# Performance work log

Measured on AMD Instinct MI355X. Metric: run time of the kernel, lower is better.

Reference implementation:

```python
import jax, jax.numpy as jnp
import numpy as np

N, D, C, E, K = 100000, 64, 40, 1600000, 2

def setup_inputs() -> dict:
    key = jax.random.key(0)
    k1, k2, k3 = jax.random.split(key, 3)
    x = jax.random.normal(k1, (N, D), dtype=jnp.float32)
    edge_index = jax.random.randint(k2, (2, E), 0, N, dtype=jnp.int64)
    W = jax.random.normal(k3, (D, C), dtype=jnp.float32) * 0.05
    b = jnp.zeros((C,), dtype=jnp.float32)
    return {"x": x, "edge_index": edge_index, "W": W, "b": b}

def reference(x, edge_index, W, b):
    n = x.shape[0]
    self_loop = jnp.arange(n, dtype=edge_index.dtype)
    row = jnp.concatenate([edge_index[0], self_loop])  # [E+N]
    col = jnp.concatenate([edge_index[1], self_loop])  # [E+N]
    # degree over row (out-degree incl. self loops), as in torch_geometric.utils.degree
    deg = jax.ops.segment_sum(jnp.ones_like(row, dtype=x.dtype), row, num_segments=n)
    deg_inv_sqrt = jnp.where(deg > 0, jax.lax.rsqrt(deg), 0.0)
    norm = deg_inv_sqrt[row] * deg_inv_sqrt[col]  # [E+N]
    # K hops of SpMM: out[r] += norm_e * x[c] for each edge e=(r,c)
    for _ in range(K):
        x = jax.ops.segment_sum(norm[:, None] * x[col], row, num_segments=n)
    logits = x @ W + b  # [N, C]
    return jax.nn.log_softmax(logits, axis=1)
```

## Files before the change

### kernel.cpp

```cpp
#include <hip/hip_runtime.h>
#include <math.h>


#define D_FEAT 64
#define NCLS 40
#define BROWS 512
#define BROWS_LOG 9
#define BINCAP 10240
#define CSRCAP 12288
#define EPT 25

__device__ __forceinline__ unsigned pack_bf16_2(float lo, float hi) {
    unsigned ulo = __float_as_uint(lo);
    unsigned uhi = __float_as_uint(hi);
    ulo = (ulo + 0x7fffu + ((ulo >> 16) & 1u)) >> 16;
    uhi = (uhi + 0x7fffu + ((uhi >> 16) & 1u)) & 0xffff0000u;
    return uhi | ulo;
}

__device__ __forceinline__ void acc2(unsigned u, float& a, float& b) {
    a += __uint_as_float(u << 16);
    b += __uint_as_float(u & 0xffff0000u);
}

__global__ void zero_cursors_kernel(int* __restrict__ cur, int nb) {
    int i = blockIdx.x * blockDim.x + threadIdx.x;
    if (i < nb) cur[i] = 0;
}

__global__ __launch_bounds__(256) void bin_edges_kernel(const int* __restrict__ rows,
                                                        const int* __restrict__ cols,
                                                        int* __restrict__ bucket_cursor,
                                                        unsigned* __restrict__ bins,
                                                        int e, int nb) {
    __shared__ int cnt[512];
    for (int i = threadIdx.x; i < nb; i += 256) cnt[i] = 0;
    __syncthreads();
    int base = blockIdx.x * (256 * EPT) + threadIdx.x;
    int rr[EPT], cc[EPT];
#pragma unroll
    for (int k = 0; k < EPT; k++) {
        int idx = base + k * 256;
        if (idx < e) { rr[k] = rows[idx]; cc[k] = cols[idx]; }
        else { rr[k] = -1; cc[k] = 0; }
    }
#pragma unroll
    for (int k = 0; k < EPT; k++)
        if (rr[k] >= 0) atomicAdd(&cnt[rr[k] >> BROWS_LOG], 1);
    __syncthreads();
    for (int i = threadIdx.x; i < nb; i += 256) {
        int c = cnt[i];
        cnt[i] = (c > 0) ? atomicAdd(&bucket_cursor[i], c) : 0;
    }
    __syncthreads();
#pragma unroll
    for (int k = 0; k < EPT; k++) {
        if (rr[k] >= 0) {
            int b = rr[k] >> BROWS_LOG;
            int pos = atomicAdd(&cnt[b], 1);
            bins[(size_t)b * BINCAP + pos] =
                ((unsigned)(rr[k] & (BROWS - 1)) << 17) | (unsigned)cc[k];
        }
    }
}

__global__ __launch_bounds__(512) void build_csr_kernel(const unsigned* __restrict__ bins,
                                                        const int* __restrict__ bucket_cursor,
                                                        int* __restrict__ csr_col,
                                                        uint2* __restrict__ row_info,
                                                        float* __restrict__ dis, int n) {
    __shared__ int cnt[512];
    __shared__ int sm[512];
    __shared__ int cur[512];
    __shared__ int lcsr[CSRCAP];
    int b = blockIdx.x;
    int tid = threadIdx.x;
    int m = bucket_cursor[b];
    cnt[tid] = 0;
    __syncthreads();
    const unsigned* bp = bins + (size_t)b * BINCAP;
    for (int i = tid; i < m; i += 512) atomicAdd(&cnt[bp[i] >> 17], 1);
    __syncthreads();
    int c = cnt[tid];
    int padded = (c + 3) & ~3;
    int r = b * BROWS + tid;
    if (r < n) dis[r] = rsqrtf(1.0f + (float)c);
    sm[tid] = padded;
    __syncthreads();
    for (int off = 1; off < 512; off <<= 1) {
        int t = (tid >= off) ? sm[tid - off] : 0;
        __syncthreads();
        sm[tid] += t;
        __syncthreads();
    }
    int off0 = sm[tid] - padded;
    cur[tid] = off0;
    if (r < n) row_info[r] = make_uint2((unsigned)(b * CSRCAP + off0), (unsigned)padded);
    __syncthreads();
    for (int i = tid; i < m; i += 512) {
        unsigned u = bp[i];
        int pos = atomicAdd(&cur[u >> 17], 1);
        lcsr[pos] = (int)(u & 0x1FFFFu);
    }
    __syncthreads();
    for (int i2 = off0 + 1; i2 < off0 + c; i2++) {
        int key = lcsr[i2];
        int j = i2 - 1;
        while (j >= off0 && lcsr[j] > key) { lcsr[j + 1] = lcsr[j]; j--; }
        lcsr[j + 1] = key;
    }
    for (int j = off0 + c; j < off0 + padded; j++) lcsr[j] = n;
    __syncthreads();
    int tot = sm[511];
    int4* cp4 = (int4*)(csr_col + (size_t)b * CSRCAP);
    const int4* l4 = (const int4*)lcsr;
    for (int i = tid; i < (tot >> 2); i += 512) cp4[i] = l4[i];
}

__global__ void scale_x_kernel(const float* __restrict__ x, const float* __restrict__ dis,
                               unsigned* __restrict__ xs0, unsigned* __restrict__ xs1, int n) {
    int i = blockIdx.x * blockDim.x + threadIdx.x;
    int total = (n + 1) * (D_FEAT / 2);
    if (i >= total) return;
    int node = i >> 5;
    if (node < n) {
        float s = dis[node];
        float2 v = ((const float2*)x)[i];
        xs0[i] = pack_bf16_2(s * v.x, s * v.y);
    } else {
        xs0[i] = 0u;
        xs1[i] = 0u;
    }
}

#define GATHER16(cp, xs_in, ql, base, len)                                  \
    uint2 u0 = make_uint2(0u, 0u), u1 = u0, u2 = u0, u3 = u0;               \
    uint2 u4 = u0, u5 = u0, u6 = u0, u7 = u0;                               \
    uint2 u8 = u0, u9 = u0, u10 = u0, u11 = u0;                             \
    uint2 u12 = u0, u13 = u0, u14 = u0, u15 = u0;                           \
    if (base < len) {                                                       \
        uint4 cv = cp[(base >> 2) + 0];                                     \
        u0 = xs_in[cv.x * 16 + ql]; u1 = xs_in[cv.y * 16 + ql];             \
        u2 = xs_in[cv.z * 16 + ql]; u3 = xs_in[cv.w * 16 + ql];             \
    }                                                                       \
    if (base + 4 < len) {                                                   \
        uint4 cv = cp[(base >> 2) + 1];                                     \
        u4 = xs_in[cv.x * 16 + ql]; u5 = xs_in[cv.y * 16 + ql];             \
        u6 = xs_in[cv.z * 16 + ql]; u7 = xs_in[cv.w * 16 + ql];             \
    }                                                                       \
    if (base + 8 < len) {                                                   \
        uint4 cv = cp[(base >> 2) + 2];                                     \
        u8 = xs_in[cv.x * 16 + ql]; u9 = xs_in[cv.y * 16 + ql];             \
        u10 = xs_in[cv.z * 16 + ql]; u11 = xs_in[cv.w * 16 + ql];           \
    }                                                                       \
    if (base + 12 < len) {                                                  \
        uint4 cv = cp[(base >> 2) + 3];                                     \
        u12 = xs_in[cv.x * 16 + ql]; u13 = xs_in[cv.y * 16 + ql];           \
        u14 = xs_in[cv.z * 16 + ql]; u15 = xs_in[cv.w * 16 + ql];           \
    }                                                                       \
    acc2(u0.x, h0, h1); acc2(u0.y, h2, h3);                                 \
    acc2(u1.x, h0, h1); acc2(u1.y, h2, h3);                                 \
    acc2(u2.x, h0, h1); acc2(u2.y, h2, h3);                                 \
    acc2(u3.x, h0, h1); acc2(u3.y, h2, h3);                                 \
    acc2(u4.x, h0, h1); acc2(u4.y, h2, h3);                                 \
    acc2(u5.x, h0, h1); acc2(u5.y, h2, h3);                                 \
    acc2(u6.x, h0, h1); acc2(u6.y, h2, h3);                                 \
    acc2(u7.x, h0, h1); acc2(u7.y, h2, h3);                                 \
    acc2(u8.x, h0, h1); acc2(u8.y, h2, h3);                                 \
    acc2(u9.x, h0, h1); acc2(u9.y, h2, h3);                                 \
    acc2(u10.x, h0, h1); acc2(u10.y, h2, h3);                               \
    acc2(u11.x, h0, h1); acc2(u11.y, h2, h3);                               \
    acc2(u12.x, h0, h1); acc2(u12.y, h2, h3);                               \
    acc2(u13.x, h0, h1); acc2(u13.y, h2, h3);                               \
    acc2(u14.x, h0, h1); acc2(u14.y, h2, h3);                               \
    acc2(u15.x, h0, h1); acc2(u15.y, h2, h3);

__global__ __launch_bounds__(256) void spmm_hop1_kernel(const uint2* __restrict__ xs_in,
                                                        uint2* __restrict__ xs_out,
                                                        const uint2* __restrict__ row_info,
                                                        const int* __restrict__ csr_col,
                                                        const float* __restrict__ dis, int n) {
    int wave = (blockIdx.x * blockDim.x + threadIdx.x) >> 6;
    int lane = threadIdx.x & 63;
    int q = lane >> 4, ql = lane & 15;
    int r = wave * 4 + q;
    bool valid = r < n;
    int s = 0, len = 0;
    if (valid) { uint2 info = row_info[r]; s = (int)info.x; len = (int)info.y; }
    int maxlen = len;
    maxlen = max(maxlen, __shfl_xor(maxlen, 16, 64));
    maxlen = max(maxlen, __shfl_xor(maxlen, 32, 64));

    float h0 = 0.f, h1 = 0.f, h2 = 0.f, h3 = 0.f;
    const uint4* cp = (const uint4*)(csr_col + s);
    for (int base = 0; base < maxlen; base += 16) {
        GATHER16(cp, xs_in, ql, base, len)
    }
    if (valid) {
        uint2 us = xs_in[r * 16 + ql];
        acc2(us.x, h0, h1); acc2(us.y, h2, h3);
        float dr = dis[r];
        float dr2 = dr * dr;
        xs_out[r * 16 + ql] = make_uint2(pack_bf16_2(dr2 * h0, dr2 * h1),
                                         pack_bf16_2(dr2 * h2, dr2 * h3));
    }
}

__global__ __launch_bounds__(256) void spmm_logits_kernel(const uint2* __restrict__ xs_in,
                                                          const uint2* __restrict__ row_info,
                                                          const int* __restrict__ csr_col,
                                                          const float* __restrict__ dis,
                                                          const float* __restrict__ W,
                                                          const float* __restrict__ b,
                                                          float* __restrict__ out, int n) {
    __shared__ float Wl[D_FEAT * NCLS];
    __shared__ float bl[NCLS];
    for (int i = threadIdx.x; i < D_FEAT * NCLS; i += blockDim.x) Wl[i] = W[i];
    for (int i = threadIdx.x; i < NCLS; i += blockDim.x) bl[i] = b[i];
    __syncthreads();

    int wave = (blockIdx.x * blockDim.x + threadIdx.x) >> 6;
    int lane = threadIdx.x & 63;
    int q = lane >> 4, ql = lane & 15;
    int r = wave * 4 + q;
    bool valid = r < n;
    int s = 0, len = 0;
    if (valid) { uint2 info = row_info[r]; s = (int)info.x; len = (int)info.y; }
    int maxlen = len;
    maxlen = max(maxlen, __shfl_xor(maxlen, 16, 64));
    maxlen = max(maxlen, __shfl_xor(maxlen, 32, 64));

    float h0 = 0.f, h1 = 0.f, h2 = 0.f, h3 = 0.f;
    const uint4* cp = (const uint4*)(csr_col + s);
    for (int base = 0; base < maxlen; base += 16) {
        GATHER16(cp, xs_in, ql, base, len)
    }

    float y0, y1, y2;
    {
        uint2 us = valid ? xs_in[r * 16 + ql] : make_uint2(0u, 0u);
        acc2(us.x, h0, h1); acc2(us.y, h2, h3);
        float dr = valid ? dis[r] : 0.f;
        h0 *= dr; h1 *= dr; h2 *= dr; h3 *= dr;

        int c0 = ql, c1 = ql + 16;
        int c2 = (ql < 8) ? (ql + 32) : ql;
        y0 = bl[c0]; y1 = bl[c1]; y2 = bl[c2];
        int qbase = q << 4;
#pragma unroll
        for (int d = 0; d < D_FEAT; d++) {
            int src = qbase + (d >> 2);
            float xv;
            switch (d & 3) {
                case 0: xv = __shfl(h0, src, 64); break;
                case 1: xv = __shfl(h1, src, 64); break;
                case 2: xv = __shfl(h2, src, 64); break;
                default: xv = __shfl(h3, src, 64); break;
            }
            y0 += xv * Wl[d * NCLS + c0];
            y1 += xv * Wl[d * NCLS + c1];
            y2 += xv * Wl[d * NCLS + c2];
        }
    }

    bool has3 = (ql < 8);
    float m = fmaxf(y0, y1);
    if (has3) m = fmaxf(m, y2);
#pragma unroll
    for (int o = 8; o > 0; o >>= 1) m = fmaxf(m, __shfl_xor(m, o, 64));
    float sm = __expf(y0 - m) + __expf(y1 - m) + (has3 ? __expf(y2 - m) : 0.f);
#pragma unroll
    for (int o = 8; o > 0; o >>= 1) sm += __shfl_xor(sm, o, 64);
    float lse = m + __logf(sm);

    if (valid) {
        float* op = out + (long long)r * NCLS;
        op[ql] = y0 - lse;
        op[ql + 16] = y1 - lse;
        if (has3) op[ql + 32] = y2 - lse;
    }
}

extern "C" void kernel_launch(void* const* d_in, const int* in_sizes, int n_in,
                              void* d_out, int out_size, void* d_ws, size_t ws_size,
                              hipStream_t stream) {
    const float* x  = (const float*)d_in[0];
    const int*   ei = (const int*)d_in[1];
    const float* W  = (const float*)d_in[2];
    const float* b  = (const float*)d_in[3];
    float* out = (float*)d_out;

    const int n = in_sizes[0] / D_FEAT;
    const int e = in_sizes[1] / 2;
    const int nb = (n + BROWS - 1) / BROWS;

    const int* rows = ei;
    const int* cols = ei + e;

    size_t na = ((size_t)n + 256) & ~(size_t)255;
    int*      bucket_cursor = (int*)d_ws;
    float*    dis           = (float*)(bucket_cursor + 256);
    uint2*    row_info      = (uint2*)(dis + na);
    unsigned* bins          = (unsigned*)(row_info + na);
    int*      csr_col       = (int*)(bins + (size_t)nb * BINCAP);
    unsigned* xs0           = (unsigned*)(csr_col + (size_t)nb * CSRCAP);
    unsigned* xs1           = xs0 + (size_t)(n + 1) * (D_FEAT / 2);

    const int BS = 256;

    zero_cursors_kernel<<<1, 256, 0, stream>>>(bucket_cursor, nb);
    {
        int blocks = (e + BS * EPT - 1) / (BS * EPT);
        bin_edges_kernel<<<blocks, BS, 0, stream>>>(rows, cols, bucket_cursor, bins, e, nb);
    }
    build_csr_kernel<<<nb, 512, 0, stream>>>(bins, bucket_cursor, csr_col, row_info, dis, n);
    {
        int tot = (n + 1) * (D_FEAT / 2);
        scale_x_kernel<<<(tot + BS - 1) / BS, BS, 0, stream>>>(x, dis, xs0, xs1, n);
    }

    int nwaves = (n + 3) / 4;
    int blocks = (nwaves * 64 + BS - 1) / BS;
    spmm_hop1_kernel<<<blocks, BS, 0, stream>>>((const uint2*)xs0, (uint2*)xs1,
                                                row_info, csr_col, dis, n);
    spmm_logits_kernel<<<blocks, BS, 0, stream>>>((const uint2*)xs1, row_info, csr_col,
                                                  dis, W, b, out, n);
}
```

Before: 242.3 us.

## Sort rows by degree within buckets, pack accumulators, stage logits matmul in LDS

build_csr_kernel now counting-sorts the rows of each 512-row bucket by padded degree and writes a permutation. Both SpMM kernels process rows in that order, so the four rows sharing a wave have similar lengths and less lane work is wasted on the max-length loop. The accumulators become packed float2 vectors to encourage packed FMA, and launch_bounds now request 6 blocks per CU. The logits projection replaces 64 cross-lane shuffles with row vectors staged in LDS and float4 reads from a transposed W, at the cost of extra shared memory and permuted output writes.

```diff
diff --git a/kernel.cpp b/kernel.cpp
--- a/kernel.cpp
+++ b/kernel.cpp
@@ -10,6 +10,8 @@
 #define CSRCAP 12288
 #define EPT 25
 
+typedef float v2f __attribute__((ext_vector_type(2)));
+
 __device__ __forceinline__ unsigned pack_bf16_2(float lo, float hi) {
     unsigned ulo = __float_as_uint(lo);
     unsigned uhi = __float_as_uint(hi);
@@ -18,9 +20,11 @@
     return uhi | ulo;
 }
 
-__device__ __forceinline__ void acc2(unsigned u, float& a, float& b) {
-    a += __uint_as_float(u << 16);
-    b += __uint_as_float(u & 0xffff0000u);
+__device__ __forceinline__ void acc2p(unsigned u, v2f& a) {
+    v2f v;
+    v.x = __uint_as_float(u << 16);
+    v.y = __uint_as_float(u & 0xffff0000u);
+    a += v;
 }
 
 __global__ void zero_cursors_kernel(int* __restrict__ cur, int nb) {
@@ -68,7 +72,8 @@
                                                         const int* __restrict__ bucket_cursor,
                                                         int* __restrict__ csr_col,
                                                         uint2* __restrict__ row_info,
-                                                        float* __restrict__ dis, int n) {
+                                                        float* __restrict__ dis,
+                                                        int* __restrict__ perm, int n) {
     __shared__ int cnt[512];
     __shared__ int sm[512];
     __shared__ int cur[512];
@@ -115,6 +120,28 @@
     int4* cp4 = (int4*)(csr_col + (size_t)b * CSRCAP);
     const int4* l4 = (const int4*)lcsr;
     for (int i = tid; i < (tot >> 2); i += 512) cp4[i] = l4[i];
+
+    if (tid < 64) cnt[tid] = 0;
+    __syncthreads();
+    int bin = min(padded >> 2, 63);
+    if (r < n) atomicAdd(&cnt[bin], 1);
+    __syncthreads();
+    if (tid < 64) sm[tid] = cnt[tid];
+    __syncthreads();
+    for (int off = 1; off < 64; off <<= 1) {
+        int t = (tid >= off && tid < 64) ? sm[tid - off] : 0;
+        __syncthreads();
+        if (tid < 64) sm[tid] += t;
+        __syncthreads();
+    }
+    if (tid < 64) cur[tid] = sm[tid] - cnt[tid];
+    __syncthreads();
+    if (r < n) {
+        int rank = atomicAdd(&cur[bin], 1);
+        perm[b * BROWS + rank] = r;
+    } else {
+        perm[b * BROWS + tid] = -1;
+    }
 }
 
 __global__ void scale_x_kernel(const float* __restrict__ x, const float* __restrict__ dis,
@@ -158,108 +185,116 @@
         u12 = xs_in[cv.x * 16 + ql]; u13 = xs_in[cv.y * 16 + ql];           \
         u14 = xs_in[cv.z * 16 + ql]; u15 = xs_in[cv.w * 16 + ql];           \
     }                                                                       \
-    acc2(u0.x, h0, h1); acc2(u0.y, h2, h3);                                 \
-    acc2(u1.x, h0, h1); acc2(u1.y, h2, h3);                                 \
-    acc2(u2.x, h0, h1); acc2(u2.y, h2, h3);                                 \
-    acc2(u3.x, h0, h1); acc2(u3.y, h2, h3);                                 \
-    acc2(u4.x, h0, h1); acc2(u4.y, h2, h3);                                 \
-    acc2(u5.x, h0, h1); acc2(u5.y, h2, h3);                                 \
-    acc2(u6.x, h0, h1); acc2(u6.y, h2, h3);                                 \
-    acc2(u7.x, h0, h1); acc2(u7.y, h2, h3);                                 \
-    acc2(u8.x, h0, h1); acc2(u8.y, h2, h3);                                 \
-    acc2(u9.x, h0, h1); acc2(u9.y, h2, h3);                                 \
-    acc2(u10.x, h0, h1); acc2(u10.y, h2, h3);                               \
-    acc2(u11.x, h0, h1); acc2(u11.y, h2, h3);                               \
-    acc2(u12.x, h0, h1); acc2(u12.y, h2, h3);                               \
-    acc2(u13.x, h0, h1); acc2(u13.y, h2, h3);                               \
-    acc2(u14.x, h0, h1); acc2(u14.y, h2, h3);                               \
-    acc2(u15.x, h0, h1); acc2(u15.y, h2, h3);
-
-__global__ __launch_bounds__(256) void spmm_hop1_kernel(const uint2* __restrict__ xs_in,
-                                                        uint2* __restrict__ xs_out,
-                                                        const uint2* __restrict__ row_info,
-                                                        const int* __restrict__ csr_col,
-                                                        const float* __restrict__ dis, int n) {
+    acc2p(u0.x, h01); acc2p(u0.y, h23);                                     \
+    acc2p(u1.x, h01); acc2p(u1.y, h23);                                     \
+    acc2p(u2.x, h01); acc2p(u2.y, h23);                                     \
+    acc2p(u3.x, h01); acc2p(u3.y, h23);                                     \
+    acc2p(u4.x, h01); acc2p(u4.y, h23);                                     \
+    acc2p(u5.x, h01); acc2p(u5.y, h23);                                     \
+    acc2p(u6.x, h01); acc2p(u6.y, h23);                                     \
+    acc2p(u7.x, h01); acc2p(u7.y, h23);                                     \
+    acc2p(u8.x, h01); acc2p(u8.y, h23);                                     \
+    acc2p(u9.x, h01); acc2p(u9.y, h23);                                     \
+    acc2p(u10.x, h01); acc2p(u10.y, h23);                                   \
+    acc2p(u11.x, h01); acc2p(u11.y, h23);                                   \
+    acc2p(u12.x, h01); acc2p(u12.y, h23);                                   \
+    acc2p(u13.x, h01); acc2p(u13.y, h23);                                   \
+    acc2p(u14.x, h01); acc2p(u14.y, h23);                                   \
+    acc2p(u15.x, h01); acc2p(u15.y, h23);
+
+__global__ __launch_bounds__(256, 6) void spmm_hop1_kernel(const uint2* __restrict__ xs_in,
+                                                           uint2* __restrict__ xs_out,
+                                                           const int* __restrict__ perm,
+                                                           const uint2* __restrict__ row_info,
+                                                           const int* __restrict__ csr_col,
+                                                           const float* __restrict__ dis,
+                                                           int n, int nperm) {
     int wave = (blockIdx.x * blockDim.x + threadIdx.x) >> 6;
     int lane = threadIdx.x & 63;
     int q = lane >> 4, ql = lane & 15;
-    int r = wave * 4 + q;
-    bool valid = r < n;
+    int pidx = wave * 4 + q;
+    int r = (pidx < nperm) ? perm[pidx] : -1;
+    bool valid = (r >= 0);
     int s = 0, len = 0;
     if (valid) { uint2 info = row_info[r]; s = (int)info.x; len = (int)info.y; }
     int maxlen = len;
     maxlen = max(maxlen, __shfl_xor(maxlen, 16, 64));
     maxlen = max(maxlen, __shfl_xor(maxlen, 32, 64));
 
-    float h0 = 0.f, h1 = 0.f, h2 = 0.f, h3 = 0.f;
+    v2f h01 = {0.f, 0.f}, h23 = {0.f, 0.f};
     const uint4* cp = (const uint4*)(csr_col + s);
     for (int base = 0; base < maxlen; base += 16) {
         GATHER16(cp, xs_in, ql, base, len)
     }
     if (valid) {
         uint2 us = xs_in[r * 16 + ql];
-        acc2(us.x, h0, h1); acc2(us.y, h2, h3);
+        acc2p(us.x, h01); acc2p(us.y, h23);
         float dr = dis[r];
         float dr2 = dr * dr;
-        xs_out[r * 16 + ql] = make_uint2(pack_bf16_2(dr2 * h0, dr2 * h1),
-                                         pack_bf16_2(dr2 * h2, dr2 * h3));
-    }
-}
-
-__global__ __launch_bounds__(256) void spmm_logits_kernel(const uint2* __restrict__ xs_in,
-                                                          const uint2* __restrict__ row_info,
-                                                          const int* __restrict__ csr_col,
-                                                          const float* __restrict__ dis,
-                                                          const float* __restrict__ W,
-                                                          const float* __restrict__ b,
-                                                          float* __restrict__ out, int n) {
-    __shared__ float Wl[D_FEAT * NCLS];
+        xs_out[r * 16 + ql] = make_uint2(pack_bf16_2(dr2 * h01.x, dr2 * h01.y),
+                                         pack_bf16_2(dr2 * h23.x, dr2 * h23.y));
+    }
+}
+
+__global__ __launch_bounds__(256, 6) void spmm_logits_kernel(const uint2* __restrict__ xs_in,
+                                                             const int* __restrict__ perm,
+                                                             const uint2* __restrict__ row_info,
+                                                             const int* __restrict__ csr_col,
+                                                             const float* __restrict__ dis,
+                                                             const float* __restrict__ W,
+                                                             const float* __restrict__ b,
+                                                             float* __restrict__ out,
+                                                             int n, int nperm) {
+    __shared__ float Wt[NCLS][D_FEAT + 4];
     __shared__ float bl[NCLS];
-    for (int i = threadIdx.x; i < D_FEAT * NCLS; i += blockDim.x) Wl[i] = W[i];
-    for (int i = threadIdx.x; i < NCLS; i += blockDim.x) bl[i] = b[i];
+    __shared__ float hl[16][D_FEAT + 4];
+    for (int i = threadIdx.x; i < D_FEAT * NCLS; i += 256) {
+        int d = i / NCLS, cc = i - d * NCLS;
+        Wt[cc][d] = W[i];
+    }
+    for (int i = threadIdx.x; i < NCLS; i += 256) bl[i] = b[i];
     __syncthreads();
 
     int wave = (blockIdx.x * blockDim.x + threadIdx.x) >> 6;
     int lane = threadIdx.x & 63;
     int q = lane >> 4, ql = lane & 15;
-    int r = wave * 4 + q;
-    bool valid = r < n;
+    int pidx = wave * 4 + q;
+    int r = (pidx < nperm) ? perm[pidx] : -1;
+    bool valid = (r >= 0);
     int s = 0, len = 0;
     if (valid) { uint2 info = row_info[r]; s = (int)info.x; len = (int)info.y; }
     int maxlen = len;
     maxlen = max(maxlen, __shfl_xor(maxlen, 16, 64));
     maxlen = max(maxlen, __shfl_xor(maxlen, 32, 64));
 
-    float h0 = 0.f, h1 = 0.f, h2 = 0.f, h3 = 0.f;
+    v2f h01 = {0.f, 0.f}, h23 = {0.f, 0.f};
     const uint4* cp = (const uint4*)(csr_col + s);
     for (int base = 0; base < maxlen; base += 16) {
         GATHER16(cp, xs_in, ql, base, len)
     }
 
     float y0, y1, y2;
+    int c0 = ql, c1 = ql + 16;
+    int c2 = (ql < 8) ? (ql + 32) : ql;
     {
         uint2 us = valid ? xs_in[r * 16 + ql] : make_uint2(0u, 0u);
-        acc2(us.x, h0, h1); acc2(us.y, h2, h3);
+        acc2p(us.x, h01); acc2p(us.y, h23);
         float dr = valid ? dis[r] : 0.f;
-        h0 *= dr; h1 *= dr; h2 *= dr; h3 *= dr;
-
-        int c0 = ql, c1 = ql + 16;
-        int c2 = (ql < 8) ? (ql + 32) : ql;
+        float h0 = h01.x * dr, h1 = h01.y * dr, h2 = h23.x * dr, h3 = h23.y * dr;
+
+        int rowslot = ((threadIdx.x >> 6) << 2) + q;
+        *(float4*)&hl[rowslot][ql * 4] = make_float4(h0, h1, h2, h3);
+
         y0 = bl[c0]; y1 = bl[c1]; y2 = bl[c2];
-        int qbase = q << 4;
-#pragma unroll
-        for (int d = 0; d < D_FEAT; d++) {
-            int src = qbase + (d >> 2);
-            float xv;
-            switch (d & 3) {
-                case 0: xv = __shfl(h0, src, 64); break;
-                case 1: xv = __shfl(h1, src, 64); break;
-                case 2: xv = __shfl(h2, src, 64); break;
-                default: xv = __shfl(h3, src, 64); break;
-            }
-            y0 += xv * Wl[d * NCLS + c0];
-            y1 += xv * Wl[d * NCLS + c1];
-            y2 += xv * Wl[d * NCLS + c2];
+#pragma unroll
+        for (int g = 0; g < 16; g++) {
+            float4 hv = *(const float4*)&hl[rowslot][g * 4];
+            float4 w0 = *(const float4*)&Wt[c0][g * 4];
+            float4 w1 = *(const float4*)&Wt[c1][g * 4];
+            float4 w2 = *(const float4*)&Wt[c2][g * 4];
+            y0 += hv.x * w0.x + hv.y * w0.y + hv.z * w0.z + hv.w * w0.w;
+            y1 += hv.x * w1.x + hv.y * w1.y + hv.z * w1.z + hv.w * w1.w;
+            y2 += hv.x * w2.x + hv.y * w2.y + hv.z * w2.z + hv.w * w2.w;
         }
     }
 
@@ -298,10 +333,12 @@
     const int* cols = ei + e;
 
     size_t na = ((size_t)n + 256) & ~(size_t)255;
+    size_t npm = (size_t)nb * BROWS;
     int*      bucket_cursor = (int*)d_ws;
     float*    dis           = (float*)(bucket_cursor + 256);
     uint2*    row_info      = (uint2*)(dis + na);
-    unsigned* bins          = (unsigned*)(row_info + na);
+    int*      perm          = (int*)(row_info + na);
+    unsigned* bins          = (unsigned*)(perm + npm);
     int*      csr_col       = (int*)(bins + (size_t)nb * BINCAP);
     unsigned* xs0           = (unsigned*)(csr_col + (size_t)nb * CSRCAP);
     unsigned* xs1           = xs0 + (size_t)(n + 1) * (D_FEAT / 2);
@@ -313,16 +350,18 @@
         int blocks = (e + BS * EPT - 1) / (BS * EPT);
         bin_edges_kernel<<<blocks, BS, 0, stream>>>(rows, cols, bucket_cursor, bins, e, nb);
     }
-    build_csr_kernel<<<nb, 512, 0, stream>>>(bins, bucket_cursor, csr_col, row_info, dis, n);
+    build_csr_kernel<<<nb, 512, 0, stream>>>(bins, bucket_cursor, csr_col, row_info, dis,
+                                             perm, n);
     {
         int tot = (n + 1) * (D_FEAT / 2);
         scale_x_kernel<<<(tot + BS - 1) / BS, BS, 0, stream>>>(x, dis, xs0, xs1, n);
     }
 
-    int nwaves = (n + 3) / 4;
+    int nperm = (int)npm;
+    int nwaves = nperm / 4;
     int blocks = (nwaves * 64 + BS - 1) / BS;
-    spmm_hop1_kernel<<<blocks, BS, 0, stream>>>((const uint2*)xs0, (uint2*)xs1,
-                                                row_info, csr_col, dis, n);
-    spmm_logits_kernel<<<blocks, BS, 0, stream>>>((const uint2*)xs1, row_info, csr_col,
-                                                  dis, W, b, out, n);
-}
+    spmm_hop1_kernel<<<blocks, BS, 0, stream>>>((const uint2*)xs0, (uint2*)xs1, perm,
+                                                row_info, csr_col, dis, n, nperm);
+    spmm_logits_kernel<<<blocks, BS, 0, stream>>>((const uint2*)xs1, perm, row_info, csr_col,
+                                                  dis, W, b, out, n, nperm);
+}
```

Result: no change. 240.9 us (-0.6%).
